# Kernel optimization log

Measured on AMD Instinct MI355X. Metric: run time of the kernel, lower is better.

Reference implementation:

```python
import jax, jax.numpy as jnp
import numpy as np

D = 256; NH = 8; NLEV = 4; NPTS = 4; DH = D // NH
DFFN = 1024; B = 8; LQ = 900
SHAPES = np.array([[100, 100], [50, 50], [25, 25], [13, 13]], dtype=np.int64)
STARTS = np.concatenate([[0], np.cumsum(SHAPES[:, 0] * SHAPES[:, 1])[:-1]]).astype(np.int64)
LEN = int((SHAPES[:, 0] * SHAPES[:, 1]).sum())


def _ln(x, w, b, eps=1e-5):
    m = x.mean(-1, keepdims=True)
    v = ((x - m) ** 2).mean(-1, keepdims=True)
    return (x - m) / jnp.sqrt(v + eps) * w + b


def _msdeform(q, ref, src, val_w, val_b, off_w, off_b, aw_w, aw_b, op_w, op_b):
    # Multi-scale deformable attention (Deformable DETR core), grid_sample
    # bilinear / zeros padding / align_corners=False semantics.
    Bq, Lq = q.shape[0], q.shape[1]
    value = (src @ val_w + val_b).reshape(Bq, -1, NH, DH)
    off = (q @ off_w + off_b).reshape(Bq, Lq, NH, NLEV, NPTS, 2)
    aw = jax.nn.softmax((q @ aw_w + aw_b).reshape(Bq, Lq, NH, NLEV * NPTS), -1)
    aw = aw.reshape(Bq, Lq, NH, NLEV, NPTS)
    norm = jnp.asarray(SHAPES[:, ::-1].copy(), dtype=q.dtype)  # (W_l, H_l)
    loc = ref[:, :, None, :, None, :] + off / norm[None, None, None, :, None, :]
    out = jnp.zeros((Bq, Lq, NH, DH), q.dtype)
    for l in range(NLEV):
        Hl, Wl = int(SHAPES[l, 0]), int(SHAPES[l, 1]); s = int(STARTS[l])
        v = value[:, s:s + Hl * Wl]                  # [B, Hl*Wl, NH, DH]
        lx = loc[:, :, :, l, :, 0] * Wl - 0.5        # align_corners=False pixel coords
        ly = loc[:, :, :, l, :, 1] * Hl - 0.5        # [B, Lq, NH, NPTS]
        x0 = jnp.floor(lx); y0 = jnp.floor(ly)
        fx = lx - x0; fy = ly - y0
        x0 = x0.astype(jnp.int32); y0 = y0.astype(jnp.int32)
        samp = jnp.zeros((Bq, Lq, NH, NPTS, DH), q.dtype)
        for dx, dy in ((0, 0), (1, 0), (0, 1), (1, 1)):
            xi = x0 + dx; yi = y0 + dy
            w = (fx if dx else 1.0 - fx) * (fy if dy else 1.0 - fy)
            valid = (xi >= 0) & (xi < Wl) & (yi >= 0) & (yi < Hl)
            idx = jnp.clip(yi, 0, Hl - 1) * Wl + jnp.clip(xi, 0, Wl - 1)
            idx_f = idx.transpose(0, 1, 3, 2).reshape(Bq, Lq * NPTS, NH)
            g = jnp.take_along_axis(v, idx_f[..., None], axis=1)
            g = g.reshape(Bq, Lq, NPTS, NH, DH).transpose(0, 1, 3, 2, 4)
            samp = samp + jnp.where(valid, w, 0.0)[..., None] * g
        out = out + jnp.sum(samp * aw[:, :, :, l, :, None], axis=3)
    return out.reshape(Bq, Lq, D) @ op_w + op_b


def _forward(tgt, query_pos, reference_points, src, qkv_w, qkv_b, out_w, out_b,
             ln2_w, ln2_b, val_w, val_b, off_w, off_b, aw_w, aw_b, op_w, op_b,
             ln1_w, ln1_b, w1, b1, w2, b2, ln3_w, ln3_b):
    Bq, Lq, _ = tgt.shape
    # --- self attention: q=k=tgt+pos, value=tgt (eval mode, no dropout) ---
    q = tgt + query_pos
    wq, wk, wv = qkv_w[:, :D], qkv_w[:, D:2 * D], qkv_w[:, 2 * D:]
    bq, bk, bv = qkv_b[:D], qkv_b[D:2 * D], qkv_b[2 * D:]
    qh = (q @ wq + bq).reshape(Bq, Lq, NH, DH)
    kh = (q @ wk + bk).reshape(Bq, Lq, NH, DH)
    vh = (tgt @ wv + bv).reshape(Bq, Lq, NH, DH)
    scores = jnp.einsum('bqhd,bkhd->bhqk', qh, kh) / jnp.sqrt(jnp.asarray(DH, tgt.dtype))
    attn = jax.nn.softmax(scores, -1)
    sa = jnp.einsum('bhqk,bkhd->bqhd', attn, vh).reshape(Bq, Lq, D) @ out_w + out_b
    tgt = _ln(tgt + sa, ln2_w, ln2_b)
    # --- multi-scale deformable cross attention ---
    ca = _msdeform(tgt + query_pos, reference_points, src,
                   val_w, val_b, off_w, off_b, aw_w, aw_b, op_w, op_b)
    tgt = _ln(tgt + ca, ln1_w, ln1_b)
    # --- FFN ---
    ff = jax.nn.relu(tgt @ w1 + b1) @ w2 + b2
    return _ln(tgt + ff, ln3_w, ln3_b)


def setup_inputs():
    key = jax.random.key(0)
    ks = jax.random.split(key, 16)
    s = 0.02
    return {
        'tgt': jax.random.normal(ks[0], (B, LQ, D), jnp.float32),
        'query_pos': jax.random.normal(ks[1], (B, LQ, D), jnp.float32),
        'reference_points': jax.random.uniform(ks[2], (B, LQ, NLEV, 2), jnp.float32),
        'src': jax.random.normal(ks[3], (B, LEN, D), jnp.float32),
        'spatial_shapes': jnp.asarray(SHAPES),
        'level_start_index': jnp.asarray(STARTS),
        'qkv_w': jax.random.normal(ks[4], (D, 3 * D), jnp.float32) * s,
        'qkv_b': jnp.zeros((3 * D,), jnp.float32),
        'out_w': jax.random.normal(ks[5], (D, D), jnp.float32) * s,
        'out_b': jnp.zeros((D,), jnp.float32),
        'ln2_w': jnp.ones((D,), jnp.float32), 'ln2_b': jnp.zeros((D,), jnp.float32),
        'val_w': jax.random.normal(ks[6], (D, D), jnp.float32) * s,
        'val_b': jnp.zeros((D,), jnp.float32),
        'off_w': jax.random.normal(ks[7], (D, NH * NLEV * NPTS * 2), jnp.float32) * s,
        'off_b': jax.random.normal(ks[8], (NH * NLEV * NPTS * 2,), jnp.float32) * 0.5,
        'aw_w': jax.random.normal(ks[9], (D, NH * NLEV * NPTS), jnp.float32) * s,
        'aw_b': jnp.zeros((NH * NLEV * NPTS,), jnp.float32),
        'op_w': jax.random.normal(ks[10], (D, D), jnp.float32) * s,
        'op_b': jnp.zeros((D,), jnp.float32),
        'ln1_w': jnp.ones((D,), jnp.float32), 'ln1_b': jnp.zeros((D,), jnp.float32),
        'w1': jax.random.normal(ks[11], (D, DFFN), jnp.float32) * s,
        'b1': jnp.zeros((DFFN,), jnp.float32),
        'w2': jax.random.normal(ks[12], (DFFN, D), jnp.float32) * s,
        'b2': jnp.zeros((D,), jnp.float32),
        'ln3_w': jnp.ones((D,), jnp.float32), 'ln3_b': jnp.zeros((D,), jnp.float32),
    }


def reference(tgt, query_pos, reference_points, src, spatial_shapes, level_start_index,
              qkv_w, qkv_b, out_w, out_b, ln2_w, ln2_b, val_w, val_b, off_w, off_b,
              aw_w, aw_b, op_w, op_b, ln1_w, ln1_b, w1, b1, w2, b2, ln3_w, ln3_b):
    return _forward(tgt, query_pos, reference_points, src, qkv_w, qkv_b, out_w, out_b,
                    ln2_w, ln2_b, val_w, val_b, off_w, off_b, aw_w, aw_b, op_w, op_b,
                    ln1_w, ln1_b, w1, b1, w2, b2, ln3_w, ln3_b)
```

## Files before the change

### kernel.cpp

```cpp
#include <hip/hip_runtime.h>
#include <math.h>

#define Dm    256
#define NHm   8
#define DHm   32
#define NLEVm 4
#define NPTSm 4
#define DFFNm 1024
#define Bm    8
#define LQm   900
#define LENm  13294
#define MQ    (Bm * LQm)
#define MV    (Bm * LENm)
#define MQP   7296
#define MVP   106368
#define LQP   960

typedef __attribute__((ext_vector_type(8))) short short8;
typedef __attribute__((ext_vector_type(4))) float f32x4;

__device__ __forceinline__ unsigned short f2bf(float f) {
    unsigned int b = __float_as_uint(f);
    unsigned int r = (b + 0x7FFFu + ((b >> 16) & 1u)) >> 16;
    return (unsigned short)r;
}
__device__ __forceinline__ float bf2f(unsigned short u) {
    return __uint_as_float(((unsigned int)u) << 16);
}

__device__ __forceinline__ void wt_tile(const float* __restrict__ W,
                                        unsigned short* __restrict__ BT,
                                        int N, int K, int n0, int k0, int t,
                                        float (*tile)[65]) {
    #pragma unroll
    for (int r0 = 0; r0 < 64; r0 += 16) {
        int r = r0 + (t >> 4);
        int c = (t & 15) * 4;
        float4 v = *reinterpret_cast<const float4*>(W + (size_t)(k0 + r) * N + n0 + c);
        tile[r][c + 0] = v.x; tile[r][c + 1] = v.y; tile[r][c + 2] = v.z; tile[r][c + 3] = v.w;
    }
    __syncthreads();
    #pragma unroll
    for (int s = t; s < 512; s += 256) {
        int r = s >> 3, c8 = (s & 7) * 8;
        short8 u;
        #pragma unroll
        for (int j = 0; j < 8; ++j) u[j] = (short)f2bf(tile[c8 + j][r]);
        *reinterpret_cast<short8*>(BT + (size_t)(n0 + r) * K + k0 + c8) = u;
    }
}

__global__ __launch_bounds__(256) void wt_prep(
        const float* __restrict__ qkv_w, const float* __restrict__ out_w,
        const float* __restrict__ val_w, const float* __restrict__ off_w,
        const float* __restrict__ aw_w,  const float* __restrict__ op_w,
        const float* __restrict__ w1,    const float* __restrict__ w2,
        unsigned short* __restrict__ BT_qkv, unsigned short* __restrict__ BT_out,
        unsigned short* __restrict__ BT_val, unsigned short* __restrict__ BT_off,
        unsigned short* __restrict__ BT_aw,  unsigned short* __restrict__ BT_op,
        unsigned short* __restrict__ BT_w1,  unsigned short* __restrict__ BT_w2,
        const float* __restrict__ tgt, const float* __restrict__ qpos,
        unsigned short* __restrict__ tgtb, unsigned short* __restrict__ qb) {
    __shared__ float tile[64][65];
    int bid = blockIdx.x;
    int t = threadIdx.x;
    if (bid >= 248) {
        int i = (bid - 248) * 256 + t;
        ushort4 ut, uq;
        if (i < MQ * 64) {
            float4 x = reinterpret_cast<const float4*>(tgt)[i];
            float4 y = reinterpret_cast<const float4*>(qpos)[i];
            ut.x = f2bf(x.x); ut.y = f2bf(x.y); ut.z = f2bf(x.z); ut.w = f2bf(x.w);
            uq.x = f2bf(x.x + y.x); uq.y = f2bf(x.y + y.y);
            uq.z = f2bf(x.z + y.z); uq.w = f2bf(x.w + y.w);
        } else {
            ut.x = ut.y = ut.z = ut.w = 0;
            uq.x = uq.y = uq.z = uq.w = 0;
        }
        reinterpret_cast<ushort4*>(tgtb)[i] = ut;
        reinterpret_cast<ushort4*>(qb)[i] = uq;
        return;
    }
    const float* W; unsigned short* BT; int N, K, idx;
    if      (bid < 48)  { W = qkv_w; BT = BT_qkv; N = 768;  K = 256;  idx = bid; }
    else if (bid < 64)  { W = out_w; BT = BT_out; N = 256;  K = 256;  idx = bid - 48; }
    else if (bid < 80)  { W = val_w; BT = BT_val; N = 256;  K = 256;  idx = bid - 64; }
    else if (bid < 96)  { W = off_w; BT = BT_off; N = 256;  K = 256;  idx = bid - 80; }
    else if (bid < 104) { W = aw_w;  BT = BT_aw;  N = 128;  K = 256;  idx = bid - 96; }
    else if (bid < 120) { W = op_w;  BT = BT_op;  N = 256;  K = 256;  idx = bid - 104; }
    else if (bid < 184) { W = w1;    BT = BT_w1;  N = 1024; K = 256;  idx = bid - 120; }
    else                { W = w2;    BT = BT_w2;  N = 256;  K = 1024; idx = bid - 184; }
    int nt = N / 64;
    int n0 = (idx % nt) * 64, k0 = (idx / nt) * 64;
    wt_tile(W, BT, N, K, n0, k0, t, tile);
}

__device__ __forceinline__ void mfma_tilestep(const unsigned short* Ac, const unsigned short* Bc,
                                              int wr, int wc, int l, f32x4 acc[4][4]) {
    short8 af[4], bfr[4];
    #pragma unroll
    for (int m = 0; m < 4; ++m)
        af[m] = *(const short8*)(Ac + (wr + m * 16 + (l & 15)) * 32 + (l >> 4) * 8);
    #pragma unroll
    for (int n = 0; n < 4; ++n)
        bfr[n] = *(const short8*)(Bc + (wc + n * 16 + (l & 15)) * 32 + (l >> 4) * 8);
    #pragma unroll
    for (int m = 0; m < 4; ++m)
        #pragma unroll
        for (int n = 0; n < 4; ++n)
            acc[m][n] = __builtin_amdgcn_mfma_f32_16x16x32_bf16(af[m], bfr[n], acc[m][n], 0, 0, 0);
}

__device__ __forceinline__ void gemm64_core(int t, unsigned short* Sh,
                                            short8& ra, short8& rb0, short8& rb1,
                                            const unsigned short* ap,
                                            const unsigned short* b0p, const unsigned short* b1p,
                                            const float* afp, f32x4 acc[2][4]) {
    int l = t & 63;
    int lr = l & 15, lg = l >> 4;
    int w = t >> 6;
    int wr = (w >> 1) * 32, wc = (w & 1) * 64;
    unsigned short* As = Sh;
    unsigned short* Bs = Sh + 2048;
    for (int k0 = 0; k0 < 256; k0 += 32) {
        __syncthreads();
        *(short8*)(As + t * 8) = ra;
        *(short8*)(Bs + t * 8) = rb0;
        *(short8*)(Bs + (t + 256) * 8) = rb1;
        __syncthreads();
        if (k0 + 32 < 256) {
            if (afp) {
                float4 f0 = *(const float4*)(afp + k0 + 32);
                float4 f1 = *(const float4*)(afp + k0 + 36);
                ra[0] = (short)f2bf(f0.x); ra[1] = (short)f2bf(f0.y);
                ra[2] = (short)f2bf(f0.z); ra[3] = (short)f2bf(f0.w);
                ra[4] = (short)f2bf(f1.x); ra[5] = (short)f2bf(f1.y);
                ra[6] = (short)f2bf(f1.z); ra[7] = (short)f2bf(f1.w);
            } else {
                ra = *(const short8*)(ap + k0 + 32);
            }
            rb0 = *(const short8*)(b0p + k0 + 32);
            rb1 = *(const short8*)(b1p + k0 + 32);
        }
        short8 af[2], bfr[4];
        #pragma unroll
        for (int m = 0; m < 2; ++m)
            af[m] = *(const short8*)(As + (wr + m * 16 + lr) * 32 + lg * 8);
        #pragma unroll
        for (int n = 0; n < 4; ++n)
            bfr[n] = *(const short8*)(Bs + (wc + n * 16 + lr) * 32 + lg * 8);
        #pragma unroll
        for (int m = 0; m < 2; ++m)
            #pragma unroll
            for (int n = 0; n < 4; ++n)
                acc[m][n] = __builtin_amdgcn_mfma_f32_16x16x32_bf16(af[m], bfr[n], acc[m][n], 0, 0, 0);
    }
}

__global__ __launch_bounds__(256) void fused_gemms(
        const float* __restrict__ src, const unsigned short* __restrict__ BT_val,
        const float* __restrict__ val_b, unsigned short* __restrict__ value_bf,
        const unsigned short* __restrict__ Qbf, const unsigned short* __restrict__ BT_qkv,
        const float* __restrict__ qkv_b, unsigned short* __restrict__ qk_bf,
        const unsigned short* __restrict__ tgt_bf, unsigned short* __restrict__ Vt) {
    __shared__ __align__(16) unsigned short Sh[6144];
    int bid = blockIdx.x;
    int t = threadIdx.x;

    if (bid >= 4008) {
        int i = (bid - 4008) * 256 + t;
        int row = i / 60, c = 900 + (i % 60);
        Vt[(size_t)row * LQP + c] = 0;
        return;
    }

    int l = t & 63, w = t >> 6;
    int lr = l & 15, lg = l >> 4;
    int wr = (w >> 1) * 32, wc = (w & 1) * 64;
    int cr = lg * 4, cc = lr;
    f32x4 acc[2][4];
    #pragma unroll
    for (int m = 0; m < 2; ++m)
        #pragma unroll
        for (int n = 0; n < 4; ++n) acc[m][n] = (f32x4){0.f, 0.f, 0.f, 0.f};

    if (bid < 3324) {
        int row0 = (bid % 1662) * 64, col0 = (bid / 1662) * 128;
        int rA = min(row0 + (t >> 2), MV - 1);
        const float* afp = src + (size_t)rA * 256 + (t & 3) * 8;
        const unsigned short* Bg = BT_val + (size_t)col0 * 256;
        const unsigned short* b0p = Bg + (size_t)(t >> 2) * 256 + (t & 3) * 8;
        const unsigned short* b1p = Bg + (size_t)((t + 256) >> 2) * 256 + ((t + 256) & 3) * 8;
        short8 ra, rb0, rb1;
        {
            float4 f0 = *(const float4*)(afp);
            float4 f1 = *(const float4*)(afp + 4);
            ra[0] = (short)f2bf(f0.x); ra[1] = (short)f2bf(f0.y);
            ra[2] = (short)f2bf(f0.z); ra[3] = (short)f2bf(f0.w);
            ra[4] = (short)f2bf(f1.x); ra[5] = (short)f2bf(f1.y);
            ra[6] = (short)f2bf(f1.z); ra[7] = (short)f2bf(f1.w);
        }
        rb0 = *(const short8*)(b0p);
        rb1 = *(const short8*)(b1p);
        gemm64_core(t, Sh, ra, rb0, rb1, nullptr, b0p, b1p, afp, acc);
        #pragma unroll
        for (int m = 0; m < 2; ++m)
            #pragma unroll
            for (int n = 0; n < 4; ++n) {
                int col = col0 + wc + n * 16 + cc;
                float bv = val_b[col];
                #pragma unroll
                for (int j = 0; j < 4; ++j) {
                    int r = row0 + wr + m * 16 + cr + j;
                    if (r < MV)
                        value_bf[(size_t)r * 256 + col] = f2bf(acc[m][n][j] + bv);
                }
            }
    } else {
        bool is_qk = (bid < 3780);
        int idx = is_qk ? (bid - 3324) : (bid - 3780);
        int row0 = (idx % 114) * 64;
        int col0 = (idx / 114) * 128;
        const unsigned short* A  = is_qk ? Qbf : tgt_bf;
        const unsigned short* BT = is_qk ? BT_qkv : (BT_qkv + 512 * 256);
        const float* bias        = is_qk ? qkv_b : (qkv_b + 512);
        const unsigned short* ap  = A  + (size_t)(row0 + (t >> 2)) * 256 + (t & 3) * 8;
        const unsigned short* Bg  = BT + (size_t)col0 * 256;
        const unsigned short* b0p = Bg + (size_t)(t >> 2) * 256 + (t & 3) * 8;
        const unsigned short* b1p = Bg + (size_t)((t + 256) >> 2) * 256 + ((t + 256) & 3) * 8;
        short8 ra = *(const short8*)(ap);
        short8 rb0 = *(const short8*)(b0p);
        short8 rb1 = *(const short8*)(b1p);
        gemm64_core(t, Sh, ra, rb0, rb1, ap, b0p, b1p, nullptr, acc);
        if (is_qk) {
            #pragma unroll
            for (int m = 0; m < 2; ++m)
                #pragma unroll
                for (int n = 0; n < 4; ++n) {
                    int col = col0 + wc + n * 16 + cc;
                    float bv = bias[col];
                    #pragma unroll
                    for (int j = 0; j < 4; ++j) {
                        int r = row0 + wr + m * 16 + cr + j;
                        if (r < MQ)
                            qk_bf[(size_t)r * 512 + col] = f2bf(acc[m][n][j] + bv);
                    }
                }
        } else {
            #pragma unroll
            for (int m = 0; m < 2; ++m)
                #pragma unroll
                for (int n = 0; n < 4; ++n) {
                    int col = col0 + wc + n * 16 + cc;
                    float bv = bias[col];
                    int r0 = row0 + wr + m * 16 + cr;
                    if (r0 < MQ) {
                        int bb = r0 / 900;
                        int q = r0 - bb * 900;
                        ushort4 u;
                        u.x = f2bf(acc[m][n][0] + bv);
                        u.y = f2bf(acc[m][n][1] + bv);
                        u.z = f2bf(acc[m][n][2] + bv);
                        u.w = f2bf(acc[m][n][3] + bv);
                        *reinterpret_cast<ushort4*>(Vt + ((size_t)(bb * 256 + col)) * LQP + q) = u;
                    }
                }
        }
    }
}

__global__ __launch_bounds__(256) void flash_mfma(const unsigned short* __restrict__ qk,
                                                  const unsigned short* __restrict__ vt,
                                                  unsigned short* __restrict__ out) {
    __shared__ unsigned short P_lds[4][16][72];
    int t = threadIdx.x;
    int l = t & 63, w = t >> 6;
    int lr = l & 15, lg = l >> 4;
    int qt = blockIdx.x, h = blockIdx.y, b = blockIdx.z;
    const float scale = 0.17677669529663687f;

    short8 qf = *(const short8*)(qk + (size_t)(b * LQm + qt * 64 + w * 16 + lr) * 512 + h * 32 + lg * 8);

    f32x4 accO[2];
    accO[0] = (f32x4){0.f, 0.f, 0.f, 0.f};
    accO[1] = (f32x4){0.f, 0.f, 0.f, 0.f};
    float mrow[4] = {-1e30f, -1e30f, -1e30f, -1e30f};
    float lrow[4] = {0.f, 0.f, 0.f, 0.f};
    const f32x4 zero = (f32x4){0.f, 0.f, 0.f, 0.f};
    const unsigned short* vtb = vt + ((size_t)(b * 256 + h * 32)) * LQP;

    for (int kt = 0; kt < 15; ++kt) {
        int k0 = kt * 64;
        f32x4 sfr[4];
        #pragma unroll
        for (int ks = 0; ks < 4; ++ks) {
            short8 kf = *(const short8*)(qk + (size_t)(b * LQm + k0 + ks * 16 + lr) * 512 + 256 + h * 32 + lg * 8);
            sfr[ks] = __builtin_amdgcn_mfma_f32_16x16x32_bf16(qf, kf, zero, 0, 0, 0);
        }
        float sv[4][4];
        #pragma unroll
        for (int ks = 0; ks < 4; ++ks) {
            bool valid = (k0 + ks * 16 + lr) < LQm;
            #pragma unroll
            for (int j = 0; j < 4; ++j)
                sv[ks][j] = valid ? sfr[ks][j] * scale : -1e30f;
        }
        float tm[4], newm[4], rr[4], ps[4];
        #pragma unroll
        for (int j = 0; j < 4; ++j)
            tm[j] = fmaxf(fmaxf(sv[0][j], sv[1][j]), fmaxf(sv[2][j], sv[3][j]));
        #pragma unroll
        for (int msk = 1; msk <= 8; msk <<= 1) {
            #pragma unroll
            for (int j = 0; j < 4; ++j) tm[j] = fmaxf(tm[j], __shfl_xor(tm[j], msk));
        }
        #pragma unroll
        for (int j = 0; j < 4; ++j) {
            newm[j] = fmaxf(mrow[j], tm[j]);
            rr[j] = __expf(mrow[j] - newm[j]);
            mrow[j] = newm[j];
            ps[j] = 0.f;
        }
        float pv[4][4];
        #pragma unroll
        for (int ks = 0; ks < 4; ++ks)
            #pragma unroll
            for (int j = 0; j < 4; ++j) {
                pv[ks][j] = __expf(sv[ks][j] - newm[j]);
                ps[j] += pv[ks][j];
            }
        #pragma unroll
        for (int msk = 1; msk <= 8; msk <<= 1) {
            #pragma unroll
            for (int j = 0; j < 4; ++j) ps[j] += __shfl_xor(ps[j], msk);
        }
        #pragma unroll
        for (int j = 0; j < 4; ++j) lrow[j] = lrow[j] * rr[j] + ps[j];
        #pragma unroll
        for (int n = 0; n < 2; ++n)
            #pragma unroll
            for (int j = 0; j < 4; ++j) accO[n][j] *= rr[j];
        #pragma unroll
        for (int ks = 0; ks < 4; ++ks)
            #pragma unroll
            for (int j = 0; j < 4; ++j)
                P_lds[w][lg * 4 + j][ks * 16 + lr] = f2bf(pv[ks][j]);
        #pragma unroll
        for (int kh2 = 0; kh2 < 2; ++kh2) {
            short8 pf = *(const short8*)(&P_lds[w][lr][kh2 * 32 + lg * 8]);
            #pragma unroll
            for (int n = 0; n < 2; ++n) {
                short8 vf = *(const short8*)(vtb + (size_t)(n * 16 + lr) * LQP + k0 + kh2 * 32 + lg * 8);
                accO[n] = __builtin_amdgcn_mfma_f32_16x16x32_bf16(pf, vf, accO[n], 0, 0, 0);
            }
        }
    }
    float inv[4];
    #pragma unroll
    for (int j = 0; j < 4; ++j) inv[j] = 1.0f / lrow[j];
    #pragma unroll
    for (int n = 0; n < 2; ++n)
        #pragma unroll
        for (int j = 0; j < 4; ++j) {
            int q = qt * 64 + w * 16 + lg * 4 + j;
            if (q < LQm)
                out[(size_t)(b * LQm + q) * 256 + h * 32 + n * 16 + lr] = f2bf(accO[n][j] * inv[j]);
        }
}

template <int RELU, int OBF>
__global__ __launch_bounds__(256) void bgemm(int M, int N, int K,
        const unsigned short* __restrict__ A,
        const unsigned short* __restrict__ BT,
        const float* __restrict__ bias, const float* __restrict__ bias2,
        float* __restrict__ Cf, float* __restrict__ Cf2,
        unsigned short* __restrict__ Cb, int ldc) {
    __shared__ __align__(16) unsigned short As[2][128 * 32];
    __shared__ __align__(16) unsigned short Bs[2][128 * 32];
    int t = threadIdx.x;
    int l = t & 63;
    int w = t >> 6;
    int row0 = blockIdx.x * 128, col0 = blockIdx.y * 128;
    int wr = (w >> 1) * 64, wc = (w & 1) * 64;
    f32x4 acc[4][4];
    #pragma unroll
    for (int m = 0; m < 4; ++m)
        #pragma unroll
        for (int n = 0; n < 4; ++n) acc[m][n] = (f32x4){0.f, 0.f, 0.f, 0.f};

    int s0 = t, s1 = t + 256;
    const unsigned short* Ag = A + (size_t)row0 * K;
    const unsigned short* Bg = BT + (size_t)col0 * K;
    const unsigned short* a0p = Ag + (size_t)(s0 >> 2) * K + (s0 & 3) * 8;
    const unsigned short* a1p = Ag + (size_t)(s1 >> 2) * K + (s1 & 3) * 8;
    const unsigned short* b0p = Bg + (size_t)(s0 >> 2) * K + (s0 & 3) * 8;
    const unsigned short* b1p = Bg + (size_t)(s1 >> 2) * K + (s1 & 3) * 8;

    short8 ra0 = *(const short8*)(a0p);
    short8 ra1 = *(const short8*)(a1p);
    short8 rb0 = *(const short8*)(b0p);
    short8 rb1 = *(const short8*)(b1p);

    int cur = 0;
    for (int k0 = 0; k0 < K; k0 += 32) {
        unsigned short* Ac = As[cur];
        unsigned short* Bc = Bs[cur];
        *(short8*)(Ac + s0 * 8) = ra0;
        *(short8*)(Ac + s1 * 8) = ra1;
        *(short8*)(Bc + s0 * 8) = rb0;
        *(short8*)(Bc + s1 * 8) = rb1;
        if (k0 + 32 < K) {
            ra0 = *(const short8*)(a0p + k0 + 32);
            ra1 = *(const short8*)(a1p + k0 + 32);
            rb0 = *(const short8*)(b0p + k0 + 32);
            rb1 = *(const short8*)(b1p + k0 + 32);
        }
        __syncthreads();
        mfma_tilestep(Ac, Bc, wr, wc, l, acc);
        cur ^= 1;
    }

    int cr = (l >> 4) * 4;
    int cc = l & 15;
    #pragma unroll
    for (int m = 0; m < 4; ++m) {
        #pragma unroll
        for (int n = 0; n < 4; ++n) {
            int col = col0 + wc + n * 16 + cc;
            if (OBF == 3) {
                float bv = (col < 256) ? bias[col] : bias2[col - 256];
                #pragma unroll
                for (int j = 0; j < 4; ++j) {
                    int r = row0 + wr + m * 16 + cr + j;
                    if (r < M) {
                        float v = acc[m][n][j] + bv;
                        if (col < 256) Cf[(size_t)r * 256 + col] = v;
                        else           Cf2[(size_t)r * 128 + (col - 256)] = v;
                    }
                }
            } else {
                float bv = bias[col];
                #pragma unroll
                for (int j = 0; j < 4; ++j) {
                    int r = row0 + wr + m * 16 + cr + j;
                    if (r < M) {
                        float v = acc[m][n][j] + bv;
                        if (RELU) v = fmaxf(v, 0.f);
                        if (OBF) Cb[(size_t)r * ldc + col] = f2bf(v);
                        else     Cf[(size_t)r * ldc + col] = v;
                    }
                }
            }
        }
    }
}

template <int DUAL, int QP>
__global__ __launch_bounds__(256) void add_ln_kernel(const float* __restrict__ x,
                                                     const float* __restrict__ r,
                                                     const float* __restrict__ w,
                                                     const float* __restrict__ b,
                                                     const float* __restrict__ qpos,
                                                     float* __restrict__ out,
                                                     unsigned short* __restrict__ outb,
                                                     unsigned short* __restrict__ outq) {
    int row = blockIdx.x * 4 + (threadIdx.x >> 6);
    int lane = threadIdx.x & 63;
    size_t i4 = (size_t)row * 64 + lane;
    float4 xv = reinterpret_cast<const float4*>(x)[i4];
    float4 rv = reinterpret_cast<const float4*>(r)[i4];
    float4 v = make_float4(xv.x + rv.x, xv.y + rv.y, xv.z + rv.z, xv.w + rv.w);
    float s = v.x + v.y + v.z + v.w;
    #pragma unroll
    for (int msk = 1; msk <= 32; msk <<= 1) s += __shfl_xor(s, msk);
    float mean = s * (1.0f / Dm);
    float4 dv = make_float4(v.x - mean, v.y - mean, v.z - mean, v.w - mean);
    float sq = dv.x * dv.x + dv.y * dv.y + dv.z * dv.z + dv.w * dv.w;
    #pragma unroll
    for (int msk = 1; msk <= 32; msk <<= 1) sq += __shfl_xor(sq, msk);
    float is = rsqrtf(sq * (1.0f / Dm) + 1e-5f);
    float4 wv = reinterpret_cast<const float4*>(w)[lane];
    float4 bv = reinterpret_cast<const float4*>(b)[lane];
    float4 res = make_float4(dv.x * is * wv.x + bv.x, dv.y * is * wv.y + bv.y,
                             dv.z * is * wv.z + bv.z, dv.w * is * wv.w + bv.w);
    reinterpret_cast<float4*>(out)[i4] = res;
    if (DUAL) {
        ushort4 u;
        u.x = f2bf(res.x); u.y = f2bf(res.y); u.z = f2bf(res.z); u.w = f2bf(res.w);
        reinterpret_cast<ushort4*>(outb)[i4] = u;
    }
    if (QP) {
        float4 qv = reinterpret_cast<const float4*>(qpos)[i4];
        ushort4 u;
        u.x = f2bf(res.x + qv.x); u.y = f2bf(res.y + qv.y);
        u.z = f2bf(res.z + qv.z); u.w = f2bf(res.w + qv.w);
        reinterpret_cast<ushort4*>(outq)[i4] = u;
    }
}

__global__ __launch_bounds__(256) void msdeform_kernel(const unsigned short* __restrict__ value,
                                                       const float* __restrict__ ref,
                                                       const float* __restrict__ off,
                                                       const float* __restrict__ awl,
                                                       unsigned short* __restrict__ out) {
    const int HL[4] = {100, 50, 25, 13};
    const int ST[4] = {0, 10000, 12500, 13125};
    __shared__ float lsx[4][128], lsy[4][128], wtab[4][128];
    __shared__ float2 ctab[4][512];
    int wv = threadIdx.x >> 6, lane = threadIdx.x & 63;
    int m = blockIdx.x * 4 + wv;
    int b = m / LQm;

    #pragma unroll
    for (int e = lane; e < 128; e += 64) {
        int lev = (e >> 2) & 3;
        float rx = ref[((size_t)m * NLEVm + lev) * 2 + 0];
        float ry = ref[((size_t)m * NLEVm + lev) * 2 + 1];
        float ox = off[(size_t)m * 256 + e * 2 + 0];
        float oy = off[(size_t)m * 256 + e * 2 + 1];
        float Wf = (float)HL[lev];
        lsx[wv][e] = (rx + ox / Wf) * Wf - 0.5f;
        lsy[wv][e] = (ry + oy / Wf) * Wf - 0.5f;
        wtab[wv][e] = awl[(size_t)m * 128 + e];
    }
    __syncthreads();
    if (lane < NHm) {
        int h = lane;
        float mx = -1e30f;
        #pragma unroll
        for (int i = 0; i < 16; i++) mx = fmaxf(mx, wtab[wv][h * 16 + i]);
        float s = 0.f;
        #pragma unroll
        for (int i = 0; i < 16; i++) {
            float e = __expf(wtab[wv][h * 16 + i] - mx);
            wtab[wv][h * 16 + i] = e; s += e;
        }
        float inv = 1.0f / s;
        #pragma unroll
        for (int i = 0; i < 16; i++) wtab[wv][h * 16 + i] *= inv;
    }
    __syncthreads();
    #pragma unroll
    for (int j = 0; j < 8; ++j) {
        int e2 = lane * 8 + j;
        int c = e2 & 3, e = e2 >> 2;
        int lev = (e >> 2) & 3;
        int Wl = HL[lev];
        float lx = lsx[wv][e], ly = lsy[wv][e];
        float x0f = floorf(lx), y0f = floorf(ly);
        float fx = lx - x0f, fy = ly - y0f;
        int dx = c & 1, dy = c >> 1;
        int xi = (int)x0f + dx, yi = (int)y0f + dy;
        bool valid = (xi >= 0) && (xi < Wl) && (yi >= 0) && (yi < Wl);
        float wc = valid ? ((dx ? fx : 1.0f - fx) * (dy ? fy : 1.0f - fy)) * wtab[wv][e] : 0.f;
        int xc = min(max(xi, 0), Wl - 1), yc = min(max(yi, 0), Wl - 1);
        int row = b * LENm + ST[lev] + yc * Wl + xc;
        ctab[wv][e2] = make_float2(__int_as_float(row), wc);
    }
    __syncthreads();
    int h = lane >> 3, dg = lane & 7;
    const unsigned short* basep = value + h * 32 + dg * 4;
    float a0 = 0.f, a1 = 0.f, a2 = 0.f, a3 = 0.f;
    #pragma unroll
    for (int i = 0; i < 16; ++i) {
        #pragma unroll
        for (int c = 0; c < 4; ++c) {
            float2 cc = ctab[wv][(h * 16 + i) * 4 + c];
            int row = __float_as_int(cc.x);
            float wc = cc.y;
            ushort4 v = *reinterpret_cast<const ushort4*>(basep + (size_t)row * 256);
            a0 += wc * bf2f(v.x); a1 += wc * bf2f(v.y);
            a2 += wc * bf2f(v.z); a3 += wc * bf2f(v.w);
        }
    }
    ushort4 o;
    o.x = f2bf(a0); o.y = f2bf(a1); o.z = f2bf(a2); o.w = f2bf(a3);
    *reinterpret_cast<ushort4*>(out + (size_t)m * 256 + h * 32 + dg * 4) = o;
}

extern "C" void kernel_launch(void* const* d_in, const int* in_sizes, int n_in,
                              void* d_out, int out_size, void* d_ws, size_t ws_size,
                              hipStream_t stream) {
    const float* tgt   = (const float*)d_in[0];
    const float* qpos  = (const float*)d_in[1];
    const float* refp  = (const float*)d_in[2];
    const float* src   = (const float*)d_in[3];
    const float* qkv_w = (const float*)d_in[6];
    const float* qkv_b = (const float*)d_in[7];
    const float* out_w = (const float*)d_in[8];
    const float* out_b = (const float*)d_in[9];
    const float* ln2_w = (const float*)d_in[10];
    const float* ln2_b = (const float*)d_in[11];
    const float* val_w = (const float*)d_in[12];
    const float* val_b = (const float*)d_in[13];
    const float* off_w = (const float*)d_in[14];
    const float* off_b = (const float*)d_in[15];
    const float* aw_w  = (const float*)d_in[16];
    const float* aw_b  = (const float*)d_in[17];
    const float* op_w  = (const float*)d_in[18];
    const float* op_b  = (const float*)d_in[19];
    const float* ln1_w = (const float*)d_in[20];
    const float* ln1_b = (const float*)d_in[21];
    const float* w1    = (const float*)d_in[22];
    const float* b1    = (const float*)d_in[23];
    const float* w2    = (const float*)d_in[24];
    const float* b2    = (const float*)d_in[25];
    const float* ln3_w = (const float*)d_in[26];
    const float* ln3_b = (const float*)d_in[27];

    char* base = (char*)d_ws;
    unsigned short* value_bf  = (unsigned short*)(base);
    unsigned short* hidden_bf = (unsigned short*)(base + 54460416);
    unsigned short* t2_bf     = (unsigned short*)(base + 54460416 + 14942208);
    unsigned short* qk_bf = (unsigned short*)(base + 108920832);
    float* offb = (float*)(base + 108920832);
    float* awb  = (float*)(base + 108920832 + 7372800);
    unsigned short* Vt = (unsigned short*)(base + 123666432);
    float* S1   = (float*)(base + 123666432);
    float* t1   = (float*)(base + 131039232);
    float* t2   = (float*)(base + 138412032);
    unsigned short* Qbf     = (unsigned short*)(base + 145784832);
    unsigned short* tgt_bf  = (unsigned short*)(base + 149520384);
    unsigned short* attn_bf = (unsigned short*)(base + 153255936);
    unsigned short* ca_bf   = (unsigned short*)(base + 156991488);
    unsigned short* BT_qkv  = (unsigned short*)(base + 160727040);
    unsigned short* BT_out  = BT_qkv + 768 * 256;
    unsigned short* BT_val  = BT_out + 256 * 256;
    unsigned short* BT_off  = BT_val + 256 * 256;
    unsigned short* BT_aw   = BT_off + 256 * 256;
    unsigned short* BT_op   = BT_aw + 128 * 256;
    unsigned short* BT_w1   = BT_op + 256 * 256;
    unsigned short* BT_w2   = BT_w1 + 1024 * 256;
    float* outp = (float*)d_out;

    dim3 blk(256);
    wt_prep<<<dim3(2072), blk, 0, stream>>>(qkv_w, out_w, val_w, off_w, aw_w, op_w, w1, w2,
                                            BT_qkv, BT_out, BT_val, BT_off, BT_aw, BT_op, BT_w1, BT_w2,
                                            tgt, qpos, tgt_bf, Qbf);
    fused_gemms<<<dim3(4488), blk, 0, stream>>>(src, BT_val, val_b, value_bf,
                                                Qbf, BT_qkv, qkv_b, qk_bf, tgt_bf, Vt);
    flash_mfma<<<dim3(15, NHm, Bm), blk, 0, stream>>>(qk_bf, Vt, attn_bf);
    bgemm<0, 0><<<dim3(57, 2), blk, 0, stream>>>(MQ, 256, 256, attn_bf, BT_out, out_b, nullptr, S1, nullptr, nullptr, 256);
    add_ln_kernel<0, 1><<<dim3(1800), blk, 0, stream>>>(tgt, S1, ln2_w, ln2_b, qpos, t1, nullptr, Qbf);
    bgemm<0, 3><<<dim3(57, 3), blk, 0, stream>>>(MQ, 384, 256, Qbf, BT_off, off_b, aw_b, offb, awb, nullptr, 0);
    msdeform_kernel<<<dim3(1800), blk, 0, stream>>>(value_bf, refp, offb, awb, ca_bf);
    bgemm<0, 0><<<dim3(57, 2), blk, 0, stream>>>(MQ, 256, 256, ca_bf, BT_op, op_b, nullptr, S1, nullptr, nullptr, 256);
    add_ln_kernel<1, 0><<<dim3(1800), blk, 0, stream>>>(t1, S1, ln1_w, ln1_b, nullptr, t2, t2_bf, nullptr);
    bgemm<1, 1><<<dim3(57, 8), blk, 0, stream>>>(MQ, DFFNm, 256, t2_bf, BT_w1, b1, nullptr, nullptr, nullptr, hidden_bf, DFFNm);
    bgemm<0, 0><<<dim3(57, 2), blk, 0, stream>>>(MQ, 256, 1024, hidden_bf, BT_w2, b2, nullptr, S1, nullptr, nullptr, 256);
    add_ln_kernel<0, 0><<<dim3(1800), blk, 0, stream>>>(t2, S1, ln3_w, ln3_b, nullptr, outp, nullptr, nullptr);
}
```

Measured before the change: 243.1 us.

## Co-schedule value projection GEMM with flash attention in one launch

Splits the old fused GEMM kernel so the QK/V projection runs first in its own launch. The value projection tiles of src then share a single launch with the flash self-attention blocks, which depend only on QK/V. The intent is to overlap the large value GEMM with the small, low-occupancy attention grid (960 blocks) and fill idle CUs. The shared LDS buffer is reused for the attention P tile. The cost is larger per-block LDS and register pressure in the merged kernel, and heterogeneous blocks in one grid.

```diff
diff --git a/kernel.cpp b/kernel.cpp
--- a/kernel.cpp
+++ b/kernel.cpp
@@ -157,127 +157,59 @@
     }
 }
 
-__global__ __launch_bounds__(256) void fused_gemms(
-        const float* __restrict__ src, const unsigned short* __restrict__ BT_val,
-        const float* __restrict__ val_b, unsigned short* __restrict__ value_bf,
-        const unsigned short* __restrict__ Qbf, const unsigned short* __restrict__ BT_qkv,
-        const float* __restrict__ qkv_b, unsigned short* __restrict__ qk_bf,
-        const unsigned short* __restrict__ tgt_bf, unsigned short* __restrict__ Vt) {
-    __shared__ __align__(16) unsigned short Sh[6144];
-    int bid = blockIdx.x;
-    int t = threadIdx.x;
-
-    if (bid >= 4008) {
-        int i = (bid - 4008) * 256 + t;
-        int row = i / 60, c = 900 + (i % 60);
-        Vt[(size_t)row * LQP + c] = 0;
-        return;
-    }
-
+__device__ __forceinline__ void value_tile64(int vbid, int t, const float* __restrict__ src,
+        const unsigned short* __restrict__ BT_val, const float* __restrict__ val_b,
+        unsigned short* __restrict__ value_bf, unsigned short* Sh) {
     int l = t & 63, w = t >> 6;
     int lr = l & 15, lg = l >> 4;
     int wr = (w >> 1) * 32, wc = (w & 1) * 64;
     int cr = lg * 4, cc = lr;
+    int row0 = (vbid % 1662) * 64, col0 = (vbid / 1662) * 128;
     f32x4 acc[2][4];
     #pragma unroll
     for (int m = 0; m < 2; ++m)
         #pragma unroll
         for (int n = 0; n < 4; ++n) acc[m][n] = (f32x4){0.f, 0.f, 0.f, 0.f};
-
-    if (bid < 3324) {
-        int row0 = (bid % 1662) * 64, col0 = (bid / 1662) * 128;
-        int rA = min(row0 + (t >> 2), MV - 1);
-        const float* afp = src + (size_t)rA * 256 + (t & 3) * 8;
-        const unsigned short* Bg = BT_val + (size_t)col0 * 256;
-        const unsigned short* b0p = Bg + (size_t)(t >> 2) * 256 + (t & 3) * 8;
-        const unsigned short* b1p = Bg + (size_t)((t + 256) >> 2) * 256 + ((t + 256) & 3) * 8;
-        short8 ra, rb0, rb1;
-        {
-            float4 f0 = *(const float4*)(afp);
-            float4 f1 = *(const float4*)(afp + 4);
-            ra[0] = (short)f2bf(f0.x); ra[1] = (short)f2bf(f0.y);
-            ra[2] = (short)f2bf(f0.z); ra[3] = (short)f2bf(f0.w);
-            ra[4] = (short)f2bf(f1.x); ra[5] = (short)f2bf(f1.y);
-            ra[6] = (short)f2bf(f1.z); ra[7] = (short)f2bf(f1.w);
-        }
-        rb0 = *(const short8*)(b0p);
-        rb1 = *(const short8*)(b1p);
-        gemm64_core(t, Sh, ra, rb0, rb1, nullptr, b0p, b1p, afp, acc);
-        #pragma unroll
-        for (int m = 0; m < 2; ++m)
-            #pragma unroll
-            for (int n = 0; n < 4; ++n) {
-                int col = col0 + wc + n * 16 + cc;
-                float bv = val_b[col];
-                #pragma unroll
-                for (int j = 0; j < 4; ++j) {
-                    int r = row0 + wr + m * 16 + cr + j;
-                    if (r < MV)
-                        value_bf[(size_t)r * 256 + col] = f2bf(acc[m][n][j] + bv);
-                }
+    int rA = min(row0 + (t >> 2), MV - 1);
+    const float* afp = src + (size_t)rA * 256 + (t & 3) * 8;
+    const unsigned short* Bg = BT_val + (size_t)col0 * 256;
+    const unsigned short* b0p = Bg + (size_t)(t >> 2) * 256 + (t & 3) * 8;
+    const unsigned short* b1p = Bg + (size_t)((t + 256) >> 2) * 256 + ((t + 256) & 3) * 8;
+    short8 ra, rb0, rb1;
+    {
+        float4 f0 = *(const float4*)(afp);
+        float4 f1 = *(const float4*)(afp + 4);
+        ra[0] = (short)f2bf(f0.x); ra[1] = (short)f2bf(f0.y);
+        ra[2] = (short)f2bf(f0.z); ra[3] = (short)f2bf(f0.w);
+        ra[4] = (short)f2bf(f1.x); ra[5] = (short)f2bf(f1.y);
+        ra[6] = (short)f2bf(f1.z); ra[7] = (short)f2bf(f1.w);
+    }
+    rb0 = *(const short8*)(b0p);
+    rb1 = *(const short8*)(b1p);
+    gemm64_core(t, Sh, ra, rb0, rb1, nullptr, b0p, b1p, afp, acc);
+    #pragma unroll
+    for (int m = 0; m < 2; ++m)
+        #pragma unroll
+        for (int n = 0; n < 4; ++n) {
+            int col = col0 + wc + n * 16 + cc;
+            float bv = val_b[col];
+            #pragma unroll
+            for (int j = 0; j < 4; ++j) {
+                int r = row0 + wr + m * 16 + cr + j;
+                if (r < MV)
+                    value_bf[(size_t)r * 256 + col] = f2bf(acc[m][n][j] + bv);
             }
-    } else {
-        bool is_qk = (bid < 3780);
-        int idx = is_qk ? (bid - 3324) : (bid - 3780);
-        int row0 = (idx % 114) * 64;
-        int col0 = (idx / 114) * 128;
-        const unsigned short* A  = is_qk ? Qbf : tgt_bf;
-        const unsigned short* BT = is_qk ? BT_qkv : (BT_qkv + 512 * 256);
-        const float* bias        = is_qk ? qkv_b : (qkv_b + 512);
-        const unsigned short* ap  = A  + (size_t)(row0 + (t >> 2)) * 256 + (t & 3) * 8;
-        const unsigned short* Bg  = BT + (size_t)col0 * 256;
-        const unsigned short* b0p = Bg + (size_t)(t >> 2) * 256 + (t & 3) * 8;
-        const unsigned short* b1p = Bg + (size_t)((t + 256) >> 2) * 256 + ((t + 256) & 3) * 8;
-        short8 ra = *(const short8*)(ap);
-        short8 rb0 = *(const short8*)(b0p);
-        short8 rb1 = *(const short8*)(b1p);
-        gemm64_core(t, Sh, ra, rb0, rb1, ap, b0p, b1p, nullptr, acc);
-        if (is_qk) {
-            #pragma unroll
-            for (int m = 0; m < 2; ++m)
-                #pragma unroll
-                for (int n = 0; n < 4; ++n) {
-                    int col = col0 + wc + n * 16 + cc;
-                    float bv = bias[col];
-                    #pragma unroll
-                    for (int j = 0; j < 4; ++j) {
-                        int r = row0 + wr + m * 16 + cr + j;
-                        if (r < MQ)
-                            qk_bf[(size_t)r * 512 + col] = f2bf(acc[m][n][j] + bv);
-                    }
-                }
-        } else {
-            #pragma unroll
-            for (int m = 0; m < 2; ++m)
-                #pragma unroll
-                for (int n = 0; n < 4; ++n) {
-                    int col = col0 + wc + n * 16 + cc;
-                    float bv = bias[col];
-                    int r0 = row0 + wr + m * 16 + cr;
-                    if (r0 < MQ) {
-                        int bb = r0 / 900;
-                        int q = r0 - bb * 900;
-                        ushort4 u;
-                        u.x = f2bf(acc[m][n][0] + bv);
-                        u.y = f2bf(acc[m][n][1] + bv);
-                        u.z = f2bf(acc[m][n][2] + bv);
-                        u.w = f2bf(acc[m][n][3] + bv);
-                        *reinterpret_cast<ushort4*>(Vt + ((size_t)(bb * 256 + col)) * LQP + q) = u;
-                    }
-                }
-        }
-    }
-}
-
-__global__ __launch_bounds__(256) void flash_mfma(const unsigned short* __restrict__ qk,
-                                                  const unsigned short* __restrict__ vt,
-                                                  unsigned short* __restrict__ out) {
-    __shared__ unsigned short P_lds[4][16][72];
-    int t = threadIdx.x;
+        }
+}
+
+__device__ __forceinline__ void flash_block(int sid, int t,
+        const unsigned short* __restrict__ qk, const unsigned short* __restrict__ vt,
+        unsigned short* __restrict__ out, unsigned short* P_lds ) {
     int l = t & 63, w = t >> 6;
     int lr = l & 15, lg = l >> 4;
-    int qt = blockIdx.x, h = blockIdx.y, b = blockIdx.z;
+    int qt = sid % 15, h = (sid / 15) % 8, b = sid / 120;
     const float scale = 0.17677669529663687f;
+    unsigned short* Pw = P_lds + w * 1152;
 
     short8 qf = *(const short8*)(qk + (size_t)(b * LQm + qt * 64 + w * 16 + lr) * 512 + h * 32 + lg * 8);
 
@@ -344,10 +276,10 @@
         for (int ks = 0; ks < 4; ++ks)
             #pragma unroll
             for (int j = 0; j < 4; ++j)
-                P_lds[w][lg * 4 + j][ks * 16 + lr] = f2bf(pv[ks][j]);
+                Pw[(lg * 4 + j) * 72 + ks * 16 + lr] = f2bf(pv[ks][j]);
         #pragma unroll
         for (int kh2 = 0; kh2 < 2; ++kh2) {
-            short8 pf = *(const short8*)(&P_lds[w][lr][kh2 * 32 + lg * 8]);
+            short8 pf = *(const short8*)(Pw + lr * 72 + kh2 * 32 + lg * 8);
             #pragma unroll
             for (int n = 0; n < 2; ++n) {
                 short8 vf = *(const short8*)(vtb + (size_t)(n * 16 + lr) * LQP + k0 + kh2 * 32 + lg * 8);
@@ -366,6 +298,95 @@
             if (q < LQm)
                 out[(size_t)(b * LQm + q) * 256 + h * 32 + n * 16 + lr] = f2bf(accO[n][j] * inv[j]);
         }
+}
+
+__global__ __launch_bounds__(256) void qkvt_kernel(
+        const unsigned short* __restrict__ Qbf, const unsigned short* __restrict__ BT_qkv,
+        const float* __restrict__ qkv_b, unsigned short* __restrict__ qk_bf,
+        const unsigned short* __restrict__ tgt_bf, unsigned short* __restrict__ Vt) {
+    __shared__ __align__(16) unsigned short Sh[6144];
+    int bid = blockIdx.x;
+    int t = threadIdx.x;
+    if (bid >= 684) {
+        int i = (bid - 684) * 256 + t;
+        int row = i / 60, c = 900 + (i % 60);
+        Vt[(size_t)row * LQP + c] = 0;
+        return;
+    }
+    int l = t & 63, w = t >> 6;
+    int lr = l & 15, lg = l >> 4;
+    int wr = (w >> 1) * 32, wc = (w & 1) * 64;
+    int cr = lg * 4, cc = lr;
+    f32x4 acc[2][4];
+    #pragma unroll
+    for (int m = 0; m < 2; ++m)
+        #pragma unroll
+        for (int n = 0; n < 4; ++n) acc[m][n] = (f32x4){0.f, 0.f, 0.f, 0.f};
+
+    bool is_qk = (bid < 456);
+    int idx = is_qk ? bid : (bid - 456);
+    int row0 = (idx % 114) * 64;
+    int col0 = (idx / 114) * 128;
+    const unsigned short* A  = is_qk ? Qbf : tgt_bf;
+    const unsigned short* BT = is_qk ? BT_qkv : (BT_qkv + 512 * 256);
+    const float* bias        = is_qk ? qkv_b : (qkv_b + 512);
+    const unsigned short* ap  = A  + (size_t)(row0 + (t >> 2)) * 256 + (t & 3) * 8;
+    const unsigned short* Bg  = BT + (size_t)col0 * 256;
+    const unsigned short* b0p = Bg + (size_t)(t >> 2) * 256 + (t & 3) * 8;
+    const unsigned short* b1p = Bg + (size_t)((t + 256) >> 2) * 256 + ((t + 256) & 3) * 8;
+    short8 ra = *(const short8*)(ap);
+    short8 rb0 = *(const short8*)(b0p);
+    short8 rb1 = *(const short8*)(b1p);
+    gemm64_core(t, Sh, ra, rb0, rb1, ap, b0p, b1p, nullptr, acc);
+    if (is_qk) {
+        #pragma unroll
+        for (int m = 0; m < 2; ++m)
+            #pragma unroll
+            for (int n = 0; n < 4; ++n) {
+                int col = col0 + wc + n * 16 + cc;
+                float bv = bias[col];
+                #pragma unroll
+                for (int j = 0; j < 4; ++j) {
+                    int r = row0 + wr + m * 16 + cr + j;
+                    if (r < MQ)
+                        qk_bf[(size_t)r * 512 + col] = f2bf(acc[m][n][j] + bv);
+                }
+            }
+    } else {
+        #pragma unroll
+        for (int m = 0; m < 2; ++m)
+            #pragma unroll
+            for (int n = 0; n < 4; ++n) {
+                int col = col0 + wc + n * 16 + cc;
+                float bv = bias[col];
+                int r0 = row0 + wr + m * 16 + cr;
+                if (r0 < MQ) {
+                    int bb = r0 / 900;
+                    int q = r0 - bb * 900;
+                    ushort4 u;
+                    u.x = f2bf(acc[m][n][0] + bv);
+                    u.y = f2bf(acc[m][n][1] + bv);
+                    u.z = f2bf(acc[m][n][2] + bv);
+                    u.w = f2bf(acc[m][n][3] + bv);
+                    *reinterpret_cast<ushort4*>(Vt + ((size_t)(bb * 256 + col)) * LQP + q) = u;
+                }
+            }
+    }
+}
+
+__global__ __launch_bounds__(256) void flash_value(
+        const unsigned short* __restrict__ qk_bf, const unsigned short* __restrict__ Vt,
+        unsigned short* __restrict__ attn_bf,
+        const float* __restrict__ src, const unsigned short* __restrict__ BT_val,
+        const float* __restrict__ val_b, unsigned short* __restrict__ value_bf) {
+    __shared__ __align__(16) unsigned short Sh[6144];
+    int bid = blockIdx.x;
+    int t = threadIdx.x;
+    if (bid < 960) {
+        flash_block(bid, t, qk_bf, Vt, attn_bf, Sh);
+    } else {
+        value_tile64(bid - 960, t, src, BT_val, val_b, value_bf, Sh);
+    }
 }
 
 template <int RELU, int OBF>
@@ -637,9 +658,8 @@
     wt_prep<<<dim3(2072), blk, 0, stream>>>(qkv_w, out_w, val_w, off_w, aw_w, op_w, w1, w2,
                                             BT_qkv, BT_out, BT_val, BT_off, BT_aw, BT_op, BT_w1, BT_w2,
                                             tgt, qpos, tgt_bf, Qbf);
-    fused_gemms<<<dim3(4488), blk, 0, stream>>>(src, BT_val, val_b, value_bf,
-                                                Qbf, BT_qkv, qkv_b, qk_bf, tgt_bf, Vt);
-    flash_mfma<<<dim3(15, NHm, Bm), blk, 0, stream>>>(qk_bf, Vt, attn_bf);
+    qkvt_kernel<<<dim3(1164), blk, 0, stream>>>(Qbf, BT_qkv, qkv_b, qk_bf, tgt_bf, Vt);
+    flash_value<<<dim3(4284), blk, 0, stream>>>(qk_bf, Vt, attn_bf, src, BT_val, val_b, value_bf);
     bgemm<0, 0><<<dim3(57, 2), blk, 0, stream>>>(MQ, 256, 256, attn_bf, BT_out, out_b, nullptr, S1, nullptr, nullptr, 256);
     add_ln_kernel<0, 1><<<dim3(1800), blk, 0, stream>>>(tgt, S1, ln2_w, ln2_b, qpos, t1, nullptr, Qbf);
     bgemm<0, 3><<<dim3(57, 3), blk, 0, stream>>>(MQ, 384, 256, Qbf, BT_off, off_b, aw_b, offb, awb, nullptr, 0);
```

After: 239.7 us, median of 3. Within noise of the previous version (-1.4%).
